# Kernel tuning notes

Hardware: AMD Instinct MI355X
Metric: run time of the kernel (lower is better)

The kernel has to match this reference:

```python
import jax, jax.numpy as jnp
import numpy as np

N_NODES = 50000


def gcn_layer(x, src, dst, W, b, norm):
    # x: [N, din]; src/dst: [E'] (self-loops included); norm: [E']
    h = x @ W                                # [N, dout]
    msg = h[src] * norm[:, None]             # [E', dout] gather + scale
    out = jax.ops.segment_sum(msg, dst, num_segments=x.shape[0])
    return out + b


def _with_self_loops_and_norm(edge_index, n):
    loop = jnp.arange(n, dtype=edge_index.dtype)
    src = jnp.concatenate([edge_index[0], loop])
    dst = jnp.concatenate([edge_index[1], loop])
    deg = jax.ops.segment_sum(jnp.ones_like(dst, dtype=jnp.float32), dst,
                              num_segments=n)
    dinv = jnp.where(deg > 0, jax.lax.rsqrt(jnp.maximum(deg, 1.0)), 0.0)
    norm = dinv[src] * dinv[dst]
    return src, dst, norm


def setup_inputs() -> dict:
    key = jax.random.key(0)
    ks = jax.random.split(key, 4)
    n, din, dh, dout = N_NODES, 128, 128, 64
    e_prev = jax.random.normal(ks[0], (n, din), dtype=jnp.float32)
    edge_index = jax.random.randint(ks[1], (2, 800000), 0, n, dtype=jnp.int64)
    W1 = jax.random.normal(ks[2], (din, dh), dtype=jnp.float32) / np.sqrt(din)
    b1 = jnp.zeros((dh,), dtype=jnp.float32)
    W2 = jax.random.normal(ks[3], (dh, dout), dtype=jnp.float32) / np.sqrt(dh)
    b2 = jnp.zeros((dout,), dtype=jnp.float32)
    return {"e_prev": e_prev, "edge_index": edge_index,
            "W1": W1, "b1": b1, "W2": W2, "b2": b2}


def reference(e_prev, edge_index, W1, b1, W2, b2):
    n = e_prev.shape[0]
    src, dst, norm = _with_self_loops_and_norm(edge_index, n)
    x = gcn_layer(e_prev, src, dst, W1, b1, norm)
    x = jax.nn.relu(x)
    x = gcn_layer(x, src, dst, W2, b2, norm)
    return x
```

## Files before the change

kernel.cpp:

```cpp
#include <hip/hip_runtime.h>
#include <hip/hip_fp16.h>


constexpr int DIN = 128;

__global__ void zero_int_k(int* __restrict__ p, int n) {
    int i = blockIdx.x * 256 + threadIdx.x;
    if (i < n) p[i] = 0;
}

__global__ void count_deg_k(const int* __restrict__ dst, int* __restrict__ cnt,
                            int* __restrict__ rank, int e) {
    int i = blockIdx.x * 256 + threadIdx.x;
    if (i < e) rank[i] = atomicAdd(&cnt[dst[i]], 1);
}

__global__ void dinv_k(const int* __restrict__ cnt, float* __restrict__ dinv, int n) {
    int i = blockIdx.x * 256 + threadIdx.x;
    if (i < n) dinv[i] = rsqrtf((float)cnt[i] + 1.0f);
}

__global__ __launch_bounds__(256) void scan1_k(const int* __restrict__ cnt,
                                               int* __restrict__ rowptr,
                                               int* __restrict__ bsum,
                                               int n_out, int n_cnt) {
    __shared__ int wsum[4];
    const int tid  = threadIdx.x;
    const int lane = tid & 63;
    const int wv   = tid >> 6;
    const int base = blockIdx.x * 1024 + tid * 4;

    int v0 = (base + 0 < n_cnt) ? cnt[base + 0] : 0;
    int v1 = (base + 1 < n_cnt) ? cnt[base + 1] : 0;
    int v2 = (base + 2 < n_cnt) ? cnt[base + 2] : 0;
    int v3 = (base + 3 < n_cnt) ? cnt[base + 3] : 0;
    int tsum = v0 + v1 + v2 + v3;

    int incl = tsum;
    for (int d = 1; d < 64; d <<= 1) {
        int t = __shfl_up(incl, d, 64);
        if (lane >= d) incl += t;
    }
    if (lane == 63) wsum[wv] = incl;
    __syncthreads();
    int woff = 0;
    for (int w = 0; w < wv; ++w) woff += wsum[w];
    int excl = woff + incl - tsum;

    int e0 = excl;
    int e1 = e0 + v0;
    int e2 = e1 + v1;
    int e3 = e2 + v2;
    if (base + 0 < n_out) rowptr[base + 0] = e0;
    if (base + 1 < n_out) rowptr[base + 1] = e1;
    if (base + 2 < n_out) rowptr[base + 2] = e2;
    if (base + 3 < n_out) rowptr[base + 3] = e3;

    if (tid == 255) bsum[blockIdx.x] = woff + incl;
}

__global__ __launch_bounds__(1024) void scan2_k(int* __restrict__ bsum, int nb) {
    __shared__ int sh[1024];
    const int t = threadIdx.x;
    int v = (t < nb) ? bsum[t] : 0;
    sh[t] = v;
    __syncthreads();
    for (int d = 1; d < 1024; d <<= 1) {
        int x = (t >= d) ? sh[t - d] : 0;
        __syncthreads();
        sh[t] += x;
        __syncthreads();
    }
    if (t < nb) bsum[t] = sh[t] - v;
}

__global__ void scan3_k(int* __restrict__ rowptr, const int* __restrict__ bsum, int n_out) {
    int i = blockIdx.x * 256 + threadIdx.x;
    if (i < n_out) rowptr[i] += bsum[i >> 10];
}

__global__ void fill_k(const int* __restrict__ src, const int* __restrict__ dst,
                       const int* __restrict__ rowptr, const int* __restrict__ rank,
                       int* __restrict__ col, int e) {
    int i = blockIdx.x * 256 + threadIdx.x;
    if (i >= e) return;
    int pos = rowptr[dst[i]] + rank[i];
    col[pos] = src[i];
}

template <int DOUT>
__global__ __launch_bounds__(256, 4) void gemm_scale_k(
    const float* __restrict__ X, const float* __restrict__ W,
    const float* __restrict__ dinv, __half* __restrict__ G, int N)
{
    constexpr int TM = 64;
    constexpr int C4 = DOUT / 4;
    constexpr int GROUPS = 256 / C4;
    constexpr int RPT = TM / GROUPS;

    __shared__ float sX[TM * DIN];

    const int tid  = threadIdx.x;
    const int base = blockIdx.x * TM;
    const float4* Wv = reinterpret_cast<const float4*>(W);

    for (int idx = tid; idx < TM * DIN / 4; idx += 256) {
        int row  = idx / (DIN / 4);
        int grow = base + row;
        float4 v = make_float4(0.f, 0.f, 0.f, 0.f);
        if (grow < N)
            v = reinterpret_cast<const float4*>(X)[(size_t)grow * (DIN / 4) + (idx % (DIN / 4))];
        reinterpret_cast<float4*>(sX)[idx] = v;
    }
    __syncthreads();

    const int cq = tid % C4;
    const int rg = tid / C4;

    float4 acc[RPT];
#pragma unroll
    for (int r = 0; r < RPT; ++r) acc[r] = make_float4(0.f, 0.f, 0.f, 0.f);

#pragma unroll 4
    for (int k = 0; k < DIN; ++k) {
        float4 w = Wv[k * C4 + cq];
#pragma unroll
        for (int r = 0; r < RPT; ++r) {
            float xv = sX[(rg + r * GROUPS) * DIN + k];
            acc[r].x = fmaf(xv, w.x, acc[r].x);
            acc[r].y = fmaf(xv, w.y, acc[r].y);
            acc[r].z = fmaf(xv, w.z, acc[r].z);
            acc[r].w = fmaf(xv, w.w, acc[r].w);
        }
    }

#pragma unroll
    for (int r = 0; r < RPT; ++r) {
        int row = base + rg + r * GROUPS;
        if (row < N) {
            float dv = dinv[row];
            __half2 p0 = __floats2half2_rn(acc[r].x * dv, acc[r].y * dv);
            __half2 p1 = __floats2half2_rn(acc[r].z * dv, acc[r].w * dv);
            uint2 packed = make_uint2(*reinterpret_cast<unsigned*>(&p0),
                                      *reinterpret_cast<unsigned*>(&p1));
            *reinterpret_cast<uint2*>(G + (size_t)row * DOUT + cq * 4) = packed;
        }
    }
}

template <int D, bool RELU>
__global__ __launch_bounds__(256) void gather_k(
    const __half* __restrict__ G, const int* __restrict__ rowptr,
    const int* __restrict__ col, const float* __restrict__ dinv,
    const float* __restrict__ bias, float* __restrict__ out, int N)
{
    constexpr int Q  = D / 8;
    constexpr int NS = 64 / Q;

    const int wave = (blockIdx.x * 256 + threadIdx.x) >> 6;
    const int lane = threadIdx.x & 63;
    if (wave >= N) return;
    const int node = wave;
    const int q    = lane % Q;
    const int slot = lane / Q;

    const uint4* G4 = reinterpret_cast<const uint4*>(G);

    float acc[8];
#pragma unroll
    for (int k = 0; k < 8; ++k) acc[k] = 0.f;

    auto accum = [&](uint4 raw) {
        const __half2* hp = reinterpret_cast<const __half2*>(&raw);
#pragma unroll
        for (int p = 0; p < 4; ++p) {
            float2 f = __half22float2(hp[p]);
            acc[2 * p]     += f.x;
            acc[2 * p + 1] += f.y;
        }
    };

    if (slot == 0) accum(G4[(size_t)node * Q + q]);
    const int beg = rowptr[node], end = rowptr[node + 1];
    int j = beg;

    for (; j + 4 * NS <= end; j += 4 * NS) {
        int s0 = col[j + 0 * NS + slot];
        int s1 = col[j + 1 * NS + slot];
        int s2 = col[j + 2 * NS + slot];
        int s3 = col[j + 3 * NS + slot];
        uint4 v0 = G4[(size_t)s0 * Q + q];
        uint4 v1 = G4[(size_t)s1 * Q + q];
        uint4 v2 = G4[(size_t)s2 * Q + q];
        uint4 v3 = G4[(size_t)s3 * Q + q];
        accum(v0); accum(v1); accum(v2); accum(v3);
    }
    for (; j + NS <= end; j += NS) {
        accum(G4[(size_t)col[j + slot] * Q + q]);
    }
    {
        int rem = end - j;
        if (slot < rem) accum(G4[(size_t)col[j + slot] * Q + q]);
    }

#pragma unroll
    for (int d = Q; d < 64; d <<= 1) {
#pragma unroll
        for (int k = 0; k < 8; ++k) acc[k] += __shfl_xor(acc[k], d, 64);
    }

    if (lane < Q) {
        float dv = dinv[node];
        float4 o0, o1;
        const float4* bb = reinterpret_cast<const float4*>(bias + q * 8);
        float4 b0 = bb[0], b1 = bb[1];
        o0.x = dv * acc[0] + b0.x;  o0.y = dv * acc[1] + b0.y;
        o0.z = dv * acc[2] + b0.z;  o0.w = dv * acc[3] + b0.w;
        o1.x = dv * acc[4] + b1.x;  o1.y = dv * acc[5] + b1.y;
        o1.z = dv * acc[6] + b1.z;  o1.w = dv * acc[7] + b1.w;
        if constexpr (RELU) {
            o0.x = fmaxf(o0.x, 0.f); o0.y = fmaxf(o0.y, 0.f);
            o0.z = fmaxf(o0.z, 0.f); o0.w = fmaxf(o0.w, 0.f);
            o1.x = fmaxf(o1.x, 0.f); o1.y = fmaxf(o1.y, 0.f);
            o1.z = fmaxf(o1.z, 0.f); o1.w = fmaxf(o1.w, 0.f);
        }
        float4* op = reinterpret_cast<float4*>(out + (size_t)node * D + q * 8);
        op[0] = o0;
        op[1] = o1;
    }
}

static inline size_t align256(size_t x) { return (x + 255) & ~size_t(255); }

extern "C" void kernel_launch(void* const* d_in, const int* in_sizes, int n_in,
                              void* d_out, int out_size, void* d_ws, size_t ws_size,
                              hipStream_t stream) {
    const float* e_prev = (const float*)d_in[0];
    const int*   eidx   = (const int*)d_in[1];
    const float* W1     = (const float*)d_in[2];
    const float* b1     = (const float*)d_in[3];
    const float* W2     = (const float*)d_in[4];
    const float* b2     = (const float*)d_in[5];

    const int dh   = in_sizes[3];
    const int din  = in_sizes[2] / dh;
    const int N    = in_sizes[0] / din;
    const int E    = in_sizes[1] / 2;
    (void)dh;

    const int* src = eidx;
    const int* dst = eidx + E;

    char* ws = (char*)d_ws;
    size_t off = 0;
    int*    cnt    = (int*)(ws + off);    off = align256(off + (size_t)N * 4);
    float*  dinv   = (float*)(ws + off);  off = align256(off + (size_t)N * 4);
    int*    rowptr = (int*)(ws + off);    off = align256(off + (size_t)(N + 1) * 4);
    int*    bsum   = (int*)(ws + off);    off = align256(off + (size_t)1024 * 4);
    int*    col    = (int*)(ws + off);    off = align256(off + (size_t)E * 4);
    int*    rank   = (int*)(ws + off);    off = align256(off + (size_t)E * 4);
    __half* gh     = (__half*)(ws + off); off = align256(off + (size_t)N * DIN * 2);
    float*  x2     = (float*)(ws + off);  off = align256(off + (size_t)N * DIN * 4);
    (void)ws_size;

    float* outp = (float*)d_out;

    const int T = 256;
    const int gN = (N + T - 1) / T;
    const int gE = (E + T - 1) / T;
    const int gW = (N + 3) / 4;
    const int n_out = N + 1;
    const int nb = (n_out + 1023) / 1024;

    zero_int_k<<<gN, T, 0, stream>>>(cnt, N);
    count_deg_k<<<gE, T, 0, stream>>>(dst, cnt, rank, E);
    dinv_k<<<gN, T, 0, stream>>>(cnt, dinv, N);
    scan1_k<<<nb, T, 0, stream>>>(cnt, rowptr, bsum, n_out, N);
    scan2_k<<<1, 1024, 0, stream>>>(bsum, nb);
    scan3_k<<<(n_out + T - 1) / T, T, 0, stream>>>(rowptr, bsum, n_out);
    fill_k<<<gE, T, 0, stream>>>(src, dst, rowptr, rank, col, E);

    gemm_scale_k<128><<<(N + 63) / 64, T, 0, stream>>>(e_prev, W1, dinv, gh, N);
    gather_k<128, true><<<gW, T, 0, stream>>>(gh, rowptr, col, dinv, b1, x2, N);

    gemm_scale_k<64><<<(N + 63) / 64, T, 0, stream>>>(x2, W2, dinv, gh, N);
    gather_k<64, false><<<gW, T, 0, stream>>>(gh, rowptr, col, dinv, b2, outp, N);
}
```

Measured before the change: 250.8 us.

## Store layer-1 activations in fp16, fuse dinv into scan, vectorise edge kernels

The layer-1 gather now writes its ReLU output as fp16, and the layer-2 GEMM reads fp16 input. This halves the traffic for the intermediate activation. The dinv computation is folded into the first scan kernel, the zeroing kernel is replaced by hipMemsetAsync, and the degree-count and CSR-fill kernels each handle two edges per thread with int2 loads. Storing the intermediate in fp16 adds rounding error, and the int2 loads assume the edge arrays are 8-byte aligned.

```diff
diff --git a/kernel.cpp b/kernel.cpp
--- a/kernel.cpp
+++ b/kernel.cpp
@@ -4,25 +4,20 @@
 
 constexpr int DIN = 128;
 
-__global__ void zero_int_k(int* __restrict__ p, int n) {
+__global__ void count_deg_k(const int* __restrict__ dst, int* __restrict__ cnt,
+                            int* __restrict__ rank, int e2, int e) {
     int i = blockIdx.x * 256 + threadIdx.x;
-    if (i < n) p[i] = 0;
-}
-
-__global__ void count_deg_k(const int* __restrict__ dst, int* __restrict__ cnt,
-                            int* __restrict__ rank, int e) {
-    int i = blockIdx.x * 256 + threadIdx.x;
-    if (i < e) rank[i] = atomicAdd(&cnt[dst[i]], 1);
-}
-
-__global__ void dinv_k(const int* __restrict__ cnt, float* __restrict__ dinv, int n) {
-    int i = blockIdx.x * 256 + threadIdx.x;
-    if (i < n) dinv[i] = rsqrtf((float)cnt[i] + 1.0f);
+    if (i >= e2) return;
+    int2 d = reinterpret_cast<const int2*>(dst)[i];
+    int r0 = atomicAdd(&cnt[d.x], 1);
+    int r1 = (2 * i + 1 < e) ? atomicAdd(&cnt[d.y], 1) : 0;
+    reinterpret_cast<int2*>(rank)[i] = make_int2(r0, r1);
 }
 
 __global__ __launch_bounds__(256) void scan1_k(const int* __restrict__ cnt,
                                                int* __restrict__ rowptr,
                                                int* __restrict__ bsum,
+                                               float* __restrict__ dinv,
                                                int n_out, int n_cnt) {
     __shared__ int wsum[4];
     const int tid  = threadIdx.x;
@@ -35,6 +30,11 @@
     int v2 = (base + 2 < n_cnt) ? cnt[base + 2] : 0;
     int v3 = (base + 3 < n_cnt) ? cnt[base + 3] : 0;
     int tsum = v0 + v1 + v2 + v3;
+
+    if (base + 0 < n_cnt) dinv[base + 0] = rsqrtf((float)v0 + 1.0f);
+    if (base + 1 < n_cnt) dinv[base + 1] = rsqrtf((float)v1 + 1.0f);
+    if (base + 2 < n_cnt) dinv[base + 2] = rsqrtf((float)v2 + 1.0f);
+    if (base + 3 < n_cnt) dinv[base + 3] = rsqrtf((float)v3 + 1.0f);
 
     int incl = tsum;
     for (int d = 1; d < 64; d <<= 1) {
@@ -81,16 +81,19 @@
 
 __global__ void fill_k(const int* __restrict__ src, const int* __restrict__ dst,
                        const int* __restrict__ rowptr, const int* __restrict__ rank,
-                       int* __restrict__ col, int e) {
+                       int* __restrict__ col, int e2, int e) {
     int i = blockIdx.x * 256 + threadIdx.x;
-    if (i >= e) return;
-    int pos = rowptr[dst[i]] + rank[i];
-    col[pos] = src[i];
-}
-
-template <int DOUT>
+    if (i >= e2) return;
+    int2 d = reinterpret_cast<const int2*>(dst)[i];
+    int2 r = reinterpret_cast<const int2*>(rank)[i];
+    int2 s = reinterpret_cast<const int2*>(src)[i];
+    col[rowptr[d.x] + r.x] = s.x;
+    if (2 * i + 1 < e) col[rowptr[d.y] + r.y] = s.y;
+}
+
+template <typename TIN, int DOUT>
 __global__ __launch_bounds__(256, 4) void gemm_scale_k(
-    const float* __restrict__ X, const float* __restrict__ W,
+    const TIN* __restrict__ X, const float* __restrict__ W,
     const float* __restrict__ dinv, __half* __restrict__ G, int N)
 {
     constexpr int TM = 64;
@@ -98,19 +101,20 @@
     constexpr int GROUPS = 256 / C4;
     constexpr int RPT = TM / GROUPS;
 
-    __shared__ float sX[TM * DIN];
+    __shared__ TIN sX[TM * DIN];
 
     const int tid  = threadIdx.x;
     const int base = blockIdx.x * TM;
     const float4* Wv = reinterpret_cast<const float4*>(W);
 
-    for (int idx = tid; idx < TM * DIN / 4; idx += 256) {
-        int row  = idx / (DIN / 4);
+    constexpr int EPL = 16 / sizeof(TIN);
+    for (int idx = tid; idx < TM * DIN / EPL; idx += 256) {
+        int row  = idx / (DIN / EPL);
         int grow = base + row;
-        float4 v = make_float4(0.f, 0.f, 0.f, 0.f);
+        uint4 v = make_uint4(0u, 0u, 0u, 0u);
         if (grow < N)
-            v = reinterpret_cast<const float4*>(X)[(size_t)grow * (DIN / 4) + (idx % (DIN / 4))];
-        reinterpret_cast<float4*>(sX)[idx] = v;
+            v = reinterpret_cast<const uint4*>(X)[(size_t)grow * (DIN / EPL) + (idx % (DIN / EPL))];
+        reinterpret_cast<uint4*>(sX)[idx] = v;
     }
     __syncthreads();
 
@@ -126,7 +130,9 @@
         float4 w = Wv[k * C4 + cq];
 #pragma unroll
         for (int r = 0; r < RPT; ++r) {
-            float xv = sX[(rg + r * GROUPS) * DIN + k];
+            float xv;
+            if constexpr (sizeof(TIN) == 4) xv = ((const float*)sX)[(rg + r * GROUPS) * DIN + k];
+            else                            xv = __half2float(((const __half*)sX)[(rg + r * GROUPS) * DIN + k]);
             acc[r].x = fmaf(xv, w.x, acc[r].x);
             acc[r].y = fmaf(xv, w.y, acc[r].y);
             acc[r].z = fmaf(xv, w.z, acc[r].z);
@@ -148,11 +154,11 @@
     }
 }
 
-template <int D, bool RELU>
+template <int D, bool RELU, typename TOUT>
 __global__ __launch_bounds__(256) void gather_k(
     const __half* __restrict__ G, const int* __restrict__ rowptr,
     const int* __restrict__ col, const float* __restrict__ dinv,
-    const float* __restrict__ bias, float* __restrict__ out, int N)
+    const float* __restrict__ bias, TOUT* __restrict__ out, int N)
 {
     constexpr int Q  = D / 8;
     constexpr int NS = 64 / Q;
@@ -211,22 +217,32 @@
 
     if (lane < Q) {
         float dv = dinv[node];
-        float4 o0, o1;
         const float4* bb = reinterpret_cast<const float4*>(bias + q * 8);
         float4 b0 = bb[0], b1 = bb[1];
-        o0.x = dv * acc[0] + b0.x;  o0.y = dv * acc[1] + b0.y;
-        o0.z = dv * acc[2] + b0.z;  o0.w = dv * acc[3] + b0.w;
-        o1.x = dv * acc[4] + b1.x;  o1.y = dv * acc[5] + b1.y;
-        o1.z = dv * acc[6] + b1.z;  o1.w = dv * acc[7] + b1.w;
+        float o[8];
+        o[0] = dv * acc[0] + b0.x;  o[1] = dv * acc[1] + b0.y;
+        o[2] = dv * acc[2] + b0.z;  o[3] = dv * acc[3] + b0.w;
+        o[4] = dv * acc[4] + b1.x;  o[5] = dv * acc[5] + b1.y;
+        o[6] = dv * acc[6] + b1.z;  o[7] = dv * acc[7] + b1.w;
         if constexpr (RELU) {
-            o0.x = fmaxf(o0.x, 0.f); o0.y = fmaxf(o0.y, 0.f);
-            o0.z = fmaxf(o0.z, 0.f); o0.w = fmaxf(o0.w, 0.f);
-            o1.x = fmaxf(o1.x, 0.f); o1.y = fmaxf(o1.y, 0.f);
-            o1.z = fmaxf(o1.z, 0.f); o1.w = fmaxf(o1.w, 0.f);
-        }
-        float4* op = reinterpret_cast<float4*>(out + (size_t)node * D + q * 8);
-        op[0] = o0;
-        op[1] = o1;
+#pragma unroll
+            for (int k = 0; k < 8; ++k) o[k] = fmaxf(o[k], 0.f);
+        }
+        if constexpr (sizeof(TOUT) == 2) {
+            __half2 h0 = __floats2half2_rn(o[0], o[1]);
+            __half2 h1 = __floats2half2_rn(o[2], o[3]);
+            __half2 h2 = __floats2half2_rn(o[4], o[5]);
+            __half2 h3 = __floats2half2_rn(o[6], o[7]);
+            uint4 packed = make_uint4(*reinterpret_cast<unsigned*>(&h0),
+                                      *reinterpret_cast<unsigned*>(&h1),
+                                      *reinterpret_cast<unsigned*>(&h2),
+                                      *reinterpret_cast<unsigned*>(&h3));
+            reinterpret_cast<uint4*>(out)[(size_t)node * Q + q] = packed;
+        } else {
+            float4* op = reinterpret_cast<float4*>((float*)out + (size_t)node * D + q * 8);
+            op[0] = make_float4(o[0], o[1], o[2], o[3]);
+            op[1] = make_float4(o[4], o[5], o[6], o[7]);
+        }
     }
 }
 
@@ -260,29 +276,29 @@
     int*    col    = (int*)(ws + off);    off = align256(off + (size_t)E * 4);
     int*    rank   = (int*)(ws + off);    off = align256(off + (size_t)E * 4);
     __half* gh     = (__half*)(ws + off); off = align256(off + (size_t)N * DIN * 2);
-    float*  x2     = (float*)(ws + off);  off = align256(off + (size_t)N * DIN * 4);
+    __half* x2h    = (__half*)(ws + off); off = align256(off + (size_t)N * DIN * 2);
     (void)ws_size;
 
     float* outp = (float*)d_out;
 
     const int T = 256;
     const int gN = (N + T - 1) / T;
-    const int gE = (E + T - 1) / T;
+    const int E2 = (E + 1) / 2;
+    const int gE2 = (E2 + T - 1) / T;
     const int gW = (N + 3) / 4;
     const int n_out = N + 1;
     const int nb = (n_out + 1023) / 1024;
 
-    zero_int_k<<<gN, T, 0, stream>>>(cnt, N);
-    count_deg_k<<<gE, T, 0, stream>>>(dst, cnt, rank, E);
-    dinv_k<<<gN, T, 0, stream>>>(cnt, dinv, N);
-    scan1_k<<<nb, T, 0, stream>>>(cnt, rowptr, bsum, n_out, N);
+    hipMemsetAsync(cnt, 0, (size_t)N * 4, stream);
+    count_deg_k<<<gE2, T, 0, stream>>>(dst, cnt, rank, E2, E);
+    scan1_k<<<nb, T, 0, stream>>>(cnt, rowptr, bsum, dinv, n_out, N);
     scan2_k<<<1, 1024, 0, stream>>>(bsum, nb);
     scan3_k<<<(n_out + T - 1) / T, T, 0, stream>>>(rowptr, bsum, n_out);
-    fill_k<<<gE, T, 0, stream>>>(src, dst, rowptr, rank, col, E);
-
-    gemm_scale_k<128><<<(N + 63) / 64, T, 0, stream>>>(e_prev, W1, dinv, gh, N);
-    gather_k<128, true><<<gW, T, 0, stream>>>(gh, rowptr, col, dinv, b1, x2, N);
-
-    gemm_scale_k<64><<<(N + 63) / 64, T, 0, stream>>>(x2, W2, dinv, gh, N);
-    gather_k<64, false><<<gW, T, 0, stream>>>(gh, rowptr, col, dinv, b2, outp, N);
-}
+    fill_k<<<gE2, T, 0, stream>>>(src, dst, rowptr, rank, col, E2, E);
+
+    gemm_scale_k<float, 128><<<(N + 63) / 64, T, 0, stream>>>(e_prev, W1, dinv, gh, N);
+    gather_k<128, true, __half><<<gW, T, 0, stream>>>(gh, rowptr, col, dinv, b1, x2h, N);
+
+    gemm_scale_k<__half, 64><<<(N + 63) / 64, T, 0, stream>>>(x2h, W2, dinv, gh, N);
+    gather_k<64, false, float><<<gW, T, 0, stream>>>(gh, rowptr, col, dinv, b2, outp, N);
+}
```

Result: faster. 245.5 us (-2.1%).
